# Performance work log

Hardware: AMD Instinct MI355X
Metric: run time of the kernel (lower is better)

The kernel has to match this reference:

```python
import jax, jax.numpy as jnp
import numpy as np

H = 64       # HIDDEN_DIM
NH = 2       # attention heads
HD = H // NH # head dim = 32
M = 8        # MEMORY_SLOTS
V = 64       # VOCAB_SIZE


def layer_norm(x, g, b):
    m = x.mean(-1, keepdims=True)
    v = ((x - m) ** 2).mean(-1, keepdims=True)
    return (x - m) / jnp.sqrt(v + 1e-5) * g + b


def mha(x, wi, bi, wo, bo):
    # torch nn.MultiheadAttention, batch_first, self-attention, avg head weights
    B, L, _ = x.shape
    qkv = x @ wi.T + bi                      # (B,L,3H)
    q, k, v = jnp.split(qkv, 3, axis=-1)
    q = q.reshape(B, L, NH, HD)
    k = k.reshape(B, L, NH, HD)
    v = v.reshape(B, L, NH, HD)
    s = jnp.einsum('bqhd,bkhd->bhqk', q, k) / jnp.sqrt(jnp.float32(HD))
    w = jax.nn.softmax(s, axis=-1)           # (B,NH,L,L)
    o = jnp.einsum('bhqk,bkhd->bqhd', w, v).reshape(B, L, H)
    return o @ wo.T + bo, w.mean(axis=1)     # averaged over heads


def ffn(x, w1, b1, w2, b2):
    return jax.nn.relu(x @ w1.T + b1) @ w2.T + b2


def setup_inputs() -> dict:
    key = jax.random.key(0)
    ks = iter(jax.random.split(key, 48))
    p = lambda shape: jax.random.normal(next(ks), shape, jnp.float32) * 0.02
    B, L = 16, 2048
    inp = {
        'seq': jax.random.randint(next(ks), (B, L), 0, V, jnp.int64 if jax.config.jax_enable_x64 else jnp.int32),
        'query': jax.random.randint(next(ks), (B,), 0, V, jnp.int32),
        'target': jax.random.randint(next(ks), (B,), 0, V, jnp.int32),
        'embed': p((V, H)),
        'a1_wi': p((3 * H, H)), 'a1_bi': p((3 * H,)), 'a1_wo': p((H, H)), 'a1_bo': p((H,)),
        'ff1_w1': p((2 * H, H)), 'ff1_b1': p((2 * H,)), 'ff1_w2': p((H, 2 * H)), 'ff1_b2': p((H,)),
        'ln1a_g': jnp.ones((H,)), 'ln1a_b': jnp.zeros((H,)),
        'ln1b_g': jnp.ones((H,)), 'ln1b_b': jnp.zeros((H,)),
        'a2_wi': p((3 * H, H)), 'a2_bi': p((3 * H,)), 'a2_wo': p((H, H)), 'a2_bo': p((H,)),
        'ff2_w1': p((2 * H, H)), 'ff2_b1': p((2 * H,)), 'ff2_w2': p((H, 2 * H)), 'ff2_b2': p((H,)),
        'ln2a_g': jnp.ones((H,)), 'ln2a_b': jnp.zeros((H,)),
        'ln2b_g': jnp.ones((H,)), 'ln2b_b': jnp.zeros((H,)),
        'rq_w': p((H, H)), 'rq_b': p((H,)),
        'ro_w': p((V, H)), 'ro_b': p((V,)),
        'qemb': p((V, H)),
    }
    return inp


def reference(seq, query, target, embed,
              a1_wi, a1_bi, a1_wo, a1_bo, ff1_w1, ff1_b1, ff1_w2, ff1_b2,
              ln1a_g, ln1a_b, ln1b_g, ln1b_b,
              a2_wi, a2_bi, a2_wo, a2_bo, ff2_w1, ff2_b1, ff2_w2, ff2_b2,
              ln2a_g, ln2a_b, ln2b_g, ln2b_b,
              rq_w, rq_b, ro_w, ro_b, qemb):
    # encoder
    h = embed[seq]                                        # (B,L,H)
    a1, _ = mha(h, a1_wi, a1_bi, a1_wo, a1_bo)
    h = layer_norm(h + a1, ln1a_g, ln1a_b)
    h = layer_norm(h + ffn(h, ff1_w1, ff1_b1, ff1_w2, ff1_b2), ln1b_g, ln1b_b)
    a2, attn_w = mha(h, a2_wi, a2_bi, a2_wo, a2_bo)       # attn_w: (B,L,L)
    h = layer_norm(h + a2, ln2a_g, ln2a_b)
    h = layer_norm(h + ffn(h, ff2_w1, ff2_b1, ff2_w2, ff2_b2), ln2b_g, ln2b_b)

    # slot selection (write_mode='attention'): per-key importance, top-k
    importance = attn_w.mean(axis=1)                      # (B,L)
    _, topk = jax.lax.top_k(importance, M)                # (B,M)
    mem = jnp.take_along_axis(h, topk[:, :, None], axis=1)  # (B,M,H)

    # memory reader
    q_h = qemb[query]                                     # (B,H)
    q = q_h @ rq_w.T + rq_b                               # (B,H)
    scores = (q[:, None, :] * mem).sum(-1) / jnp.sqrt(jnp.float32(H))  # (B,M)
    weights = jax.nn.softmax(scores, axis=-1)[:, :, None]
    read = (weights * mem).sum(1)                         # (B,H)
    logits = read @ ro_w.T + ro_b                         # (B,V)

    logp = jax.nn.log_softmax(logits, axis=-1)
    loss = -jnp.mean(logp[jnp.arange(logits.shape[0]), target])
    return loss, attn_w
```

## Files before the change

### kernel.cpp

```cpp
#include <hip/hip_runtime.h>
#include <hip/hip_bf16.h>


typedef unsigned short u16;
#define LQ 2048
#define BBATCH 16
#define QKB 262144

typedef __attribute__((ext_vector_type(8))) short bf16x8;
typedef __attribute__((ext_vector_type(4))) float f32x4;

__device__ __forceinline__ float bfu2f(u16 x){ return __uint_as_float(((unsigned)x) << 16); }
__device__ __forceinline__ u16 f2bu(float f){ return __bfloat16_as_ushort(__float2bfloat16(f)); }

__device__ __forceinline__ unsigned cvtpk(float lo, float hi){
  unsigned r;
  asm("v_cvt_pk_bf16_f32 %0, %1, %2" : "=v"(r) : "v"(lo), "v"(hi));
  return r;
}

__device__ __forceinline__ const u16* qk_rowp(const u16* qk_r15, const u16* qk_ws,
                                              int bz, int row){
  const u16* base = (bz < 15) ? (qk_r15 + (size_t)bz*QKB) : qk_ws;
  return base + (size_t)row*128;
}
__device__ __forceinline__ u16* qk_rowp_w(u16* qk_r15, u16* qk_ws, int bz, int row){
  u16* base = (bz < 15) ? (qk_r15 + (size_t)bz*QKB) : qk_ws;
  return base + (size_t)row*128;
}

__global__ __launch_bounds__(256) void k_embed(const int* __restrict__ seq,
                                               const float* __restrict__ emb,
                                               u16* __restrict__ h){
  int i = blockIdx.x*256 + threadIdx.x;
  int tok = i >> 6, d = i & 63;
  int v = seq[tok] & 63;
  h[i] = f2bu(emb[(v << 6) + d]);
}

__global__ __launch_bounds__(256) void k_zero(float* __restrict__ p, float* __restrict__ q){
  int i = blockIdx.x*256 + threadIdx.x;
  p[i] = 0.f;
  if (i == 0) q[0] = 0.f;
}

template<int MODE>
__global__ __launch_bounds__(256) void k_qkv(const u16* __restrict__ X,
                                             const float* __restrict__ W,
                                             const float* __restrict__ bias,
                                             u16* __restrict__ dqk0,
                                             u16* __restrict__ dqk_r15,
                                             u16* __restrict__ dqk_ws,
                                             u16* __restrict__ vg){
  __shared__ float WT[64*193];
  __shared__ float bs[192];
  const int t = threadIdx.x;
  for (int e=t; e<192*64; e+=256){ int mo=e>>6, k=e&63; WT[k*193+mo] = W[e]; }
  if (t < 192) bs[t] = bias[t];
  __syncthreads();
  const int wid=t>>6, lane=t&63;
  const int tok0 = (blockIdx.x*4 + wid)*4;
  float x[4];
  #pragma unroll
  for (int c=0;c<4;c++) x[c] = bfu2f(X[(tok0+c)*64 + lane]);
  float acc[4][3];
  #pragma unroll
  for (int c=0;c<4;c++)
    #pragma unroll
    for (int m=0;m<3;m++) acc[c][m] = bs[m*64 + lane];
  for (int k=0;k<64;k++){
    float wv[3];
    #pragma unroll
    for (int m=0;m<3;m++) wv[m] = WT[k*193 + m*64 + lane];
    #pragma unroll
    for (int c=0;c<4;c++){
      float xk = __shfl(x[c], k);
      #pragma unroll
      for (int m=0;m<3;m++) acc[c][m] += xk*wv[m];
    }
  }
  const float qs = 0.17677669529663688f;
  #pragma unroll
  for (int c=0;c<4;c++){
    int tok = tok0+c;
    float vq = acc[c][0]*qs, vk = acc[c][1], vv = acc[c][2];
    int b = tok >> 11, r = tok & 2047;
    u16* row = (MODE==0) ? (dqk0 + (size_t)tok*128) : qk_rowp_w(dqk_r15, dqk_ws, b, r);
    row[lane]      = f2bu(vq);
    row[64 + lane] = f2bu(vk);
    vg[((size_t)((b*64 + (r>>5))*4 + ((r>>2)&3))*64 + lane)*8
       + ((r>>4)&1)*4 + (r&3)] = f2bu(vv);
  }
}

template<int MODE>
__global__ __launch_bounds__(256, 4) void k_attn_ln(const u16* __restrict__ PQK,
    const u16* __restrict__ QKWS, const u16* __restrict__ VG,
    const float* __restrict__ wo, const float* __restrict__ bo,
    const float* __restrict__ g, const float* __restrict__ be,
    u16* __restrict__ h, float* __restrict__ lout){
  __shared__ float R[4096];
  __shared__ float ST[32*68];
  __shared__ float DN[2][32];
  __shared__ float CB[192];
  const int lin = blockIdx.x;
  const int nid = (lin & 7)*128 + (lin >> 3);
  const int qt = nid & 63, bz = nid >> 6;
  const int t = threadIdx.x;
  const int lane = t & 63, wv = t >> 6;
  const int n = lane & 15, gq = lane >> 4;
  const f32x4 FZ = {0.f, 0.f, 0.f, 0.f};

  for (int e=t; e<2048; e+=256) R[e] = 0.f;
  if (t < 64) DN[t>>5][t&31] = 0.f;
  __syncthreads();

  bf16x8 qf[2][2];
  #pragma unroll
  for (int qa=0; qa<2; qa++){
    const u16* qrow = (MODE==0) ? (PQK + (size_t)(bz*LQ + qt*32 + qa*16 + n)*128)
                                : qk_rowp(PQK, QKWS, bz, qt*32 + qa*16 + n);
    qf[qa][0] = *(const bf16x8*)(qrow + gq*8);
    qf[qa][1] = *(const bf16x8*)(qrow + 32 + gq*8);
  }
  f32x4 o[2][2][2];
  #pragma unroll
  for (int qa=0; qa<2; qa++)
    #pragma unroll
    for (int hh=0; hh<2; hh++)
      #pragma unroll
      for (int db=0; db<2; db++) o[qa][hh][db] = FZ;
  float dacc[2][2] = {{0.f,0.f},{0.f,0.f}};

  #pragma unroll 1
  for (int kt=wv*8; kt<wv*8+8; kt++){
    #pragma unroll
    for (int hh=0; hh<2; hh++){
      bf16x8 kf[4];
      #pragma unroll
      for (int jb=0; jb<4; jb++){
        const u16* kr = (MODE==0) ? (PQK + (size_t)(bz*LQ + kt*64 + jb*16 + n)*128)
                                  : qk_rowp(PQK, QKWS, bz, kt*64 + jb*16 + n);
        kf[jb] = *(const bf16x8*)(kr + 64 + hh*32 + gq*8);
      }
      unsigned pk[2][4][2];
      #pragma unroll
      for (int qa=0; qa<2; qa++){
        f32x4 ev[4];
        #pragma unroll
        for (int jb=0; jb<4; jb++)
          ev[jb] = __builtin_amdgcn_mfma_f32_16x16x32_bf16(kf[jb], qf[qa][hh], FZ, 0, 0, 0);
        float ds = 0.f;
        #pragma unroll
        for (int jb=0; jb<4; jb++){
          float e0 = __expf(ev[jb][0]), e1 = __expf(ev[jb][1]);
          float e2 = __expf(ev[jb][2]), e3 = __expf(ev[jb][3]);
          ds += (e0+e1) + (e2+e3);
          pk[qa][jb][0] = cvtpk(e0, e1);
          pk[qa][jb][1] = cvtpk(e2, e3);
        }
        dacc[qa][hh] += ds;
      }
      #pragma unroll
      for (int kb=0; kb<2; kb++){
        union { unsigned u[4]; bf16x8 v; } af[2];
        #pragma unroll
        for (int qa=0; qa<2; qa++){
          af[qa].u[0] = pk[qa][2*kb][0];   af[qa].u[1] = pk[qa][2*kb][1];
          af[qa].u[2] = pk[qa][2*kb+1][0]; af[qa].u[3] = pk[qa][2*kb+1][1];
        }
        #pragma unroll
        for (int db=0; db<2; db++){
          const int d = hh*32 + db*16 + n;
          const bf16x8 vf = *(const bf16x8*)(VG +
              ((size_t)((bz*64 + kt*2 + kb)*4 + gq)*64 + d)*8);
          #pragma unroll
          for (int qa=0; qa<2; qa++)
            o[qa][hh][db] = __builtin_amdgcn_mfma_f32_16x16x32_bf16(af[qa].v, vf, o[qa][hh][db], 0, 0, 0);
        }
      }
    }
  }
  #pragma unroll
  for (int qa=0; qa<2; qa++)
    #pragma unroll
    for (int hh=0; hh<2; hh++){
      float s = dacc[qa][hh];
      s += __shfl_xor(s, 16);
      s += __shfl_xor(s, 32);
      if (gq == 0) atomicAdd(&DN[hh][qa*16 + n], s);
    }
  #pragma unroll
  for (int qa=0; qa<2; qa++)
    #pragma unroll
    for (int hh=0; hh<2; hh++)
      #pragma unroll
      for (int db=0; db<2; db++)
        #pragma unroll
        for (int r=0; r<4; r++)
          atomicAdd(&R[(qa*16 + gq*4 + r)*64 + hh*32 + db*16 + n], o[qa][hh][db][r]);
  __syncthreads();
  if (lout && t < 64)
    lout[(size_t)(bz*2 + (t>>5))*LQ + qt*32 + (t&31)] = DN[t>>5][t&31];
  for (int e=t; e<2048; e+=256){
    int q = e >> 6, d = e & 63;
    ST[q*68 + d] = R[e] / DN[d>>5][q];
  }
  __syncthreads();
  for (int e2=t; e2<4096; e2+=256){ int k=e2>>6, mo=e2&63; R[e2] = wo[mo*64+k]; }
  if (t < 64)       CB[t] = bo[t];
  else if (t < 128) CB[t] = g[t-64];
  else if (t < 192) CB[t] = be[t-128];
  __syncthreads();
  for (int r=0; r<8; r++){
    int tl = wv*8 + r;
    size_t gtok = (size_t)(bz*LQ + qt*32 + tl);
    float acc = CB[lane];
    for (int k=0; k<64; k++) acc += ST[tl*68 + k] * R[k*64 + lane];
    float rr = acc + bfu2f(h[gtok*64 + lane]);
    float s = rr;
    #pragma unroll
    for (int ofs=32; ofs; ofs>>=1) s += __shfl_xor(s, ofs);
    float mean = s * (1.f/64.f);
    float dv = rr - mean;
    float vs = dv*dv;
    #pragma unroll
    for (int ofs=32; ofs; ofs>>=1) vs += __shfl_xor(vs, ofs);
    float rstd = 1.f/sqrtf(vs*(1.f/64.f) + 1e-5f);
    h[gtok*64 + lane] = f2bu(dv*rstd*CB[64+lane] + CB[128+lane]);
  }
}

__global__ __launch_bounds__(256) void k_ffn(u16* __restrict__ h,
    const float* __restrict__ w1, const float* __restrict__ b1,
    const float* __restrict__ w2, const float* __restrict__ b2,
    const float* __restrict__ g, const float* __restrict__ be){
  __shared__ u16 W1L[128*64];
  __shared__ u16 W2L[64*192];
  __shared__ u16 YL[64*64];
  __shared__ float B1[128], B2F[64], G[64], Bb[64];
  const int t = threadIdx.x;
  for (int e=t; e<8192; e+=256){
    int row = e>>6, col = e&63;
    W1L[row*64 + (col ^ ((row&7)<<3))] = f2bu(w1[e]);
  }
  for (int e=t; e<12288; e+=256){
    int o = e/192, rem = e%192, u = rem>>5, gs = rem&31, gq2 = gs>>3, s = gs&7;
    float val;
    if (u < 4) val = w2[o*128 + u*32 + ((s>>2)<<4) + gq2*4 + (s&3)];
    else { int d = ((u-4)<<5) + gq2*8 + s; val = (d==o) ? 1.f : 0.f; }
    W2L[o*192 + ((u*32+gs) ^ ((o&7)<<3))] = f2bu(val);
  }
  if (t < 128) B1[t] = b1[t];
  if (t < 64){ B2F[t] = b2[t]; G[t] = g[t]; Bb[t] = be[t]; }
  __syncthreads();
  const int lane = t & 63, wv = t >> 6;
  const int n = lane & 15, gq = lane >> 4;
  const int tok0 = blockIdx.x*64 + wv*16;
  bf16x8 xf[2];
  xf[0] = *(const bf16x8*)(h + (size_t)(tok0+n)*64 + gq*8);
  xf[1] = *(const bf16x8*)(h + (size_t)(tok0+n)*64 + 32 + gq*8);
  f32x4 acc1[8];
  #pragma unroll
  for (int ct=0; ct<8; ct++){
    f32x4 c;
    #pragma unroll
    for (int r=0;r<4;r++) c[r] = B1[ct*16 + gq*4 + r];
    bf16x8 w1f0 = *(const bf16x8*)(W1L + (ct*16+n)*64 + ((gq*8) ^ ((n&7)<<3)));
    bf16x8 w1f1 = *(const bf16x8*)(W1L + (ct*16+n)*64 + ((32+gq*8) ^ ((n&7)<<3)));
    c = __builtin_amdgcn_mfma_f32_16x16x32_bf16(w1f0, xf[0], c, 0, 0, 0);
    c = __builtin_amdgcn_mfma_f32_16x16x32_bf16(w1f1, xf[1], c, 0, 0, 0);
    acc1[ct] = c;
  }
  f32x4 acc2[4];
  #pragma unroll
  for (int ot=0; ot<4; ot++)
    #pragma unroll
    for (int r=0;r<4;r++) acc2[ot][r] = B2F[ot*16 + gq*4 + r];
  #pragma unroll
  for (int u=0; u<6; u++){
    union { unsigned uu[4]; bf16x8 v; } bfr;
    if (u < 4){
      #pragma unroll
      for (int i=0;i<4;i++){
        int ct = u*2 + (i>>1);
        float a = fmaxf(acc1[ct][(2*i)&3], 0.f);
        float b = fmaxf(acc1[ct][(2*i+1)&3], 0.f);
        bfr.uu[i] = (unsigned)f2bu(a) | ((unsigned)f2bu(b) << 16);
      }
    } else {
      bfr.v = xf[u-4];
    }
    #pragma unroll
    for (int ot=0; ot<4; ot++){
      bf16x8 w2f = *(const bf16x8*)(W2L + (ot*16+n)*192 + ((u*32+gq*8) ^ ((n&7)<<3)));
      acc2[ot] = __builtin_amdgcn_mfma_f32_16x16x32_bf16(w2f, bfr.v, acc2[ot], 0, 0, 0);
    }
  }
  float s1 = 0.f;
  #pragma unroll
  for (int ot=0;ot<4;ot++)
    #pragma unroll
    for (int r=0;r<4;r++) s1 += acc2[ot][r];
  s1 += __shfl_xor(s1, 16); s1 += __shfl_xor(s1, 32);
  float mean = s1 * (1.f/64.f);
  float s2 = 0.f;
  #pragma unroll
  for (int ot=0;ot<4;ot++)
    #pragma unroll
    for (int r=0;r<4;r++){ float dv = acc2[ot][r]-mean; s2 += dv*dv; }
  s2 += __shfl_xor(s2, 16); s2 += __shfl_xor(s2, 32);
  float rstd = 1.f/sqrtf(s2*(1.f/64.f) + 1e-5f);
  #pragma unroll
  for (int ot=0;ot<4;ot++)
    #pragma unroll
    for (int r=0;r<4;r++){
      int o = ot*16 + gq*4 + r;
      float yv = (acc2[ot][r]-mean)*rstd*G[o] + Bb[o];
      YL[(wv*16+n)*64 + (o ^ ((n&7)<<3))] = f2bu(yv);
    }
  __syncthreads();
  unsigned* h32 = (unsigned*)(h + (size_t)(blockIdx.x)*64*64);
  #pragma unroll
  for (int i=0;i<8;i++){
    int idx = i*64 + lane;
    int row = wv*16 + (idx>>5), c32 = idx&31;
    unsigned vv = *(const unsigned*)(YL + row*64 + ((c32*2) ^ ((row&7)<<3)));
    h32[row*32 + c32] = vv;
  }
}

__global__ __launch_bounds__(256) void k_imp(const u16* __restrict__ qk_r15,
    const u16* __restrict__ qk_ws, const float* __restrict__ l2,
    float* __restrict__ imp, int bz0){
  __shared__ float IMPS[256];
  __shared__ float INVL[128];
  const int t = threadIdx.x;
  const int qt = blockIdx.x >> 3, ks = blockIdx.x & 7;
  const int bz = bz0;
  const int lane = t & 63, wv = t >> 6;
  const int n = lane & 15, gq = lane >> 4;
  const f32x4 FZ = {0.f, 0.f, 0.f, 0.f};
  if (t < 128) INVL[t] = 1.f / l2[(size_t)(bz*2 + (t>>6))*LQ + qt*64 + (t&63)];
  IMPS[t] = 0.f;
  bf16x8 qf0, qf1;
  {
    const u16* qrow = qk_rowp(qk_r15, qk_ws, bz, qt*64 + wv*16 + n);
    qf0 = *(const bf16x8*)(qrow + gq*8);
    qf1 = *(const bf16x8*)(qrow + 32 + gq*8);
  }
  __syncthreads();
  float iv0[4], iv1[4];
  #pragma unroll
  for (int r=0;r<4;r++){
    iv0[r] = INVL[wv*16 + gq*4 + r];
    iv1[r] = INVL[64 + wv*16 + gq*4 + r];
  }
  for (int kt=ks*4; kt<ks*4+4; kt++){
    #pragma unroll
    for (int jb=0; jb<4; jb++){
      const u16* kr = qk_rowp(qk_r15, qk_ws, bz, kt*64 + jb*16 + n);
      bf16x8 kf0 = *(const bf16x8*)(kr + 64 + gq*8);
      bf16x8 kf1 = *(const bf16x8*)(kr + 96 + gq*8);
      f32x4 e0 = __builtin_amdgcn_mfma_f32_16x16x32_bf16(qf0, kf0, FZ, 0, 0, 0);
      f32x4 e1 = __builtin_amdgcn_mfma_f32_16x16x32_bf16(qf1, kf1, FZ, 0, 0, 0);
      float cs = 0.f;
      #pragma unroll
      for (int r=0;r<4;r++)
        cs += 0.5f*(__expf(e0[r])*iv0[r] + __expf(e1[r])*iv1[r]);
      cs += __shfl_xor(cs, 16);
      cs += __shfl_xor(cs, 32);
      if (gq == 0) atomicAdd(&IMPS[(kt-ks*4)*64 + jb*16 + n], cs);
    }
  }
  __syncthreads();
  atomicAdd(&imp[bz*LQ + ks*256 + t], IMPS[t]);
}

template<int DOIMP>
__global__ __launch_bounds__(256) void k_pass2(const u16* __restrict__ qk_r15,
    const u16* __restrict__ qk_ws, const float* __restrict__ l2,
    float* __restrict__ imp, float* __restrict__ wout, int bz0, int nper){
  __shared__ float STG[64*68];
  __shared__ float INVL[128];
  const int x = blockIdx.x;
  const int nid = (x & 7)*nper + (x >> 3);
  const int bz = bz0 + (nid >> 8);
  const int rem = nid & 255;
  const int qt = rem >> 3, ks = rem & 7;
  const int t = threadIdx.x;
  const int lane = t & 63, wv = t >> 6;
  const int n = lane & 15, gq = lane >> 4;
  const f32x4 FZ = {0.f, 0.f, 0.f, 0.f};
  if (t < 128) INVL[t] = 1.f / l2[(size_t)(bz*2 + (t>>6))*LQ + qt*64 + (t&63)];
  bf16x8 qf0, qf1;
  {
    const u16* qrow = qk_rowp(qk_r15, qk_ws, bz, qt*64 + wv*16 + n);
    qf0 = *(const bf16x8*)(qrow + gq*8);
    qf1 = *(const bf16x8*)(qrow + 32 + gq*8);
  }
  __syncthreads();
  const float iv0 = INVL[wv*16 + n], iv1 = INVL[64 + wv*16 + n];
  for (int kt = ks*4; kt < ks*4 + 4; kt++){
    #pragma unroll
    for (int jb=0; jb<4; jb++){
      const u16* kr = qk_rowp(qk_r15, qk_ws, bz, kt*64 + jb*16 + n);
      bf16x8 kf0 = *(const bf16x8*)(kr + 64 + gq*8);
      bf16x8 kf1 = *(const bf16x8*)(kr + 96 + gq*8);
      f32x4 e0 = __builtin_amdgcn_mfma_f32_16x16x32_bf16(kf0, qf0, FZ, 0, 0, 0);
      f32x4 e1 = __builtin_amdgcn_mfma_f32_16x16x32_bf16(kf1, qf1, FZ, 0, 0, 0);
      float4 w4;
      w4.x = 0.5f*(__expf(e0[0])*iv0 + __expf(e1[0])*iv1);
      w4.y = 0.5f*(__expf(e0[1])*iv0 + __expf(e1[1])*iv1);
      w4.z = 0.5f*(__expf(e0[2])*iv0 + __expf(e1[2])*iv1);
      w4.w = 0.5f*(__expf(e0[3])*iv0 + __expf(e1[3])*iv1);
      *(float4*)(&STG[(wv*16 + n)*68 + jb*16 + 4*gq]) = w4;
    }
    size_t base = 1 + (size_t)bz*LQ*LQ + (size_t)(qt*64)*LQ + (size_t)kt*64;
    float p = 0.f;
    for (int r=0; r<16; r++){
      int q = wv*16 + r;
      float v = STG[q*68 + lane];
      wout[base + (size_t)q*LQ + lane] = v;
      p += v;
    }
    if (DOIMP) atomicAdd(&imp[bz*LQ + kt*64 + lane], p);
  }
}

__global__ __launch_bounds__(64) void k_select(const float* __restrict__ imp,
    const u16* __restrict__ h,
    const int* __restrict__ query, const int* __restrict__ target,
    const float* __restrict__ qemb, const float* __restrict__ rq_w, const float* __restrict__ rq_b,
    const float* __restrict__ ro_w, const float* __restrict__ ro_b, float* __restrict__ out0){
  __shared__ float v[2048];
  __shared__ float bv[64];
  __shared__ int   bi[64];
  __shared__ int   chosen;
  __shared__ int   topi[8];
  const int b = blockIdx.x, lane = threadIdx.x;
  for (int i=lane; i<2048; i+=64) v[i] = imp[b*2048 + i];
  __syncthreads();
  for (int m=0; m<8; m++){
    float best = -1e30f; int besti = 1<<30;
    for (int i=lane; i<2048; i+=64)
      if (v[i] > best || (v[i] == best && i < besti)){ best = v[i]; besti = i; }
    bv[lane] = best; bi[lane] = besti;
    __syncthreads();
    if (lane == 0){
      float B = bv[0]; int I = bi[0];
      for (int i2=1; i2<64; i2++)
        if (bv[i2] > B || (bv[i2] == B && bi[i2] < I)){ B = bv[i2]; I = bi[i2]; }
      int c = (I < 0) ? 0 : (I > 2047 ? 2047 : I);
      topi[m] = c;
      chosen = c;
    }
    __syncthreads();
    if (lane == 0) v[chosen] = -1e30f;
    __syncthreads();
  }
  float mv[8];
  #pragma unroll
  for (int m=0; m<8; m++){
    int idx = topi[m] & 2047;
    mv[m] = bfu2f(h[(size_t)(b*LQ + idx)*64 + lane]);
  }
  float qh = qemb[((query[b]&63)<<6) + lane];
  float qd = rq_b[lane];
  for (int k=0;k<64;k++) qd += __shfl(qh,k) * rq_w[lane*64 + k];
  float sc[8];
  #pragma unroll
  for (int m=0;m<8;m++){
    float p = qd * mv[m];
    #pragma unroll
    for (int o=32;o;o>>=1) p += __shfl_xor(p,o);
    sc[m] = p * 0.125f;
  }
  float mx = sc[0];
  #pragma unroll
  for (int m=1;m<8;m++) mx = fmaxf(mx, sc[m]);
  float den = 0.f, rd = 0.f;
  #pragma unroll
  for (int m=0;m<8;m++){ float w = __expf(sc[m]-mx); den += w; rd += w*mv[m]; }
  rd /= den;
  float lg = ro_b[lane];
  for (int d=0;d<64;d++) lg += __shfl(rd,d) * ro_w[lane*64 + d];
  float lmx = lg;
  #pragma unroll
  for (int o=32;o;o>>=1) lmx = fmaxf(lmx, __shfl_xor(lmx,o));
  float ex = __expf(lg - lmx), es = ex;
  #pragma unroll
  for (int o=32;o;o>>=1) es += __shfl_xor(es,o);
  float lt = __shfl(lg, target[b]&63);
  if (lane == 0) atomicAdd(out0, -(lt - lmx - logf(es)) * (1.f/16.f));
}

extern "C" void kernel_launch(void* const* d_in, const int* in_sizes, int n_in,
                              void* d_out, int out_size, void* d_ws, size_t ws_size,
                              hipStream_t stream){
  const int*   seq    = (const int*)  d_in[0];
  const int*   query  = (const int*)  d_in[1];
  const int*   target = (const int*)  d_in[2];
  const float* embed  = (const float*)d_in[3];
  const float* a1_wi  = (const float*)d_in[4];
  const float* a1_bi  = (const float*)d_in[5];
  const float* a1_wo  = (const float*)d_in[6];
  const float* a1_bo  = (const float*)d_in[7];
  const float* ff1_w1 = (const float*)d_in[8];
  const float* ff1_b1 = (const float*)d_in[9];
  const float* ff1_w2 = (const float*)d_in[10];
  const float* ff1_b2 = (const float*)d_in[11];
  const float* ln1a_g = (const float*)d_in[12];
  const float* ln1a_b = (const float*)d_in[13];
  const float* ln1b_g = (const float*)d_in[14];
  const float* ln1b_b = (const float*)d_in[15];
  const float* a2_wi  = (const float*)d_in[16];
  const float* a2_bi  = (const float*)d_in[17];
  const float* a2_wo  = (const float*)d_in[18];
  const float* a2_bo  = (const float*)d_in[19];
  const float* ff2_w1 = (const float*)d_in[20];
  const float* ff2_b1 = (const float*)d_in[21];
  const float* ff2_w2 = (const float*)d_in[22];
  const float* ff2_b2 = (const float*)d_in[23];
  const float* ln2a_g = (const float*)d_in[24];
  const float* ln2a_b = (const float*)d_in[25];
  const float* ln2b_g = (const float*)d_in[26];
  const float* ln2b_b = (const float*)d_in[27];
  const float* rq_w   = (const float*)d_in[28];
  const float* rq_b   = (const float*)d_in[29];
  const float* ro_w   = (const float*)d_in[30];
  const float* ro_b   = (const float*)d_in[31];
  const float* qemb   = (const float*)d_in[32];

  char* wsb      = (char*)d_ws;
  u16*  qk_ws    = (u16*)(wsb);
  float* ws_imp  = (float*)(wsb + 524288);
  float* ws_l    = (float*)(wsb + 655360);

  float* out_f  = (float*)d_out;
  u16* qk1     = (u16*)((char*)d_out + 4194368);
  u16* vg1     = (u16*)((char*)d_out + 12582976);
  u16* vg2     = (u16*)((char*)d_out + 4194368);
  u16* qk_r15  = (u16*)((char*)d_out + 251658304);
  u16* h16     = (u16*)((char*)d_out + 259522624);

  k_embed<<<8192,256,0,stream>>>(seq, embed, h16);
  k_zero<<<128,256,0,stream>>>(ws_imp, out_f);
  k_qkv<0><<<2048,256,0,stream>>>(h16, a1_wi, a1_bi, qk1, nullptr, nullptr, vg1);
  k_attn_ln<0><<<1024,256,0,stream>>>(qk1, nullptr, vg1,
                                      a1_wo, a1_bo, ln1a_g, ln1a_b, h16, nullptr);
  k_ffn<<<512,256,0,stream>>>(h16, ff1_w1, ff1_b1, ff1_w2, ff1_b2, ln1b_g, ln1b_b);
  k_qkv<1><<<2048,256,0,stream>>>(h16, a2_wi, a2_bi, nullptr, qk_r15, qk_ws, vg2);
  k_attn_ln<1><<<1024,256,0,stream>>>(qk_r15, qk_ws, vg2,
                                      a2_wo, a2_bo, ln2a_g, ln2a_b, h16, ws_l);
  k_ffn<<<512,256,0,stream>>>(h16, ff2_w1, ff2_b1, ff2_w2, ff2_b2, ln2b_g, ln2b_b);
  k_pass2<1><<<3840,256,0,stream>>>(qk_r15, qk_ws, ws_l, ws_imp, out_f, 0, 480);
  k_imp<<<256,256,0,stream>>>(qk_r15, qk_ws, ws_l, ws_imp, 15);
  k_select<<<16,64,0,stream>>>(ws_imp, h16, query, target, qemb,
                               rq_w, rq_b, ro_w, ro_b, out_f);
  k_pass2<0><<<256,256,0,stream>>>(qk_r15, qk_ws, ws_l, nullptr, out_f, 15, 32);
}
```

Measured before the change: 838.1 us.

## Use MFMA for QKV projection, fold zeroing into embed, partial importance sums

The QKV projection moves from a scalar FMA loop with shuffles to bf16 MFMA tiles of 64 tokens per block. Output is staged in LDS so Q/K rows and the V layout can be written with wider coalesced stores. The zero-init kernel is merged into the embed kernel. In pass2, importance partials accumulate in shared memory and go to a per-query-tile buffer that k_select reduces, replacing global atomics. The attention-weight stores become nontemporal. Risks: bf16 rounding of weights, and extra reads in k_select.

```diff
diff --git a/kernel.cpp b/kernel.cpp
--- a/kernel.cpp
+++ b/kernel.cpp
@@ -31,17 +31,15 @@
 
 __global__ __launch_bounds__(256) void k_embed(const int* __restrict__ seq,
                                                const float* __restrict__ emb,
-                                               u16* __restrict__ h){
+                                               u16* __restrict__ h,
+                                               float* __restrict__ imp0,
+                                               float* __restrict__ out0){
   int i = blockIdx.x*256 + threadIdx.x;
+  if (i < 32768) imp0[i] = 0.f;
+  if (i == 0) out0[0] = 0.f;
   int tok = i >> 6, d = i & 63;
   int v = seq[tok] & 63;
   h[i] = f2bu(emb[(v << 6) + d]);
-}
-
-__global__ __launch_bounds__(256) void k_zero(float* __restrict__ p, float* __restrict__ q){
-  int i = blockIdx.x*256 + threadIdx.x;
-  p[i] = 0.f;
-  if (i == 0) q[0] = 0.f;
 }
 
 template<int MODE>
@@ -52,44 +50,62 @@
                                              u16* __restrict__ dqk_r15,
                                              u16* __restrict__ dqk_ws,
                                              u16* __restrict__ vg){
-  __shared__ float WT[64*193];
-  __shared__ float bs[192];
+  __shared__ u16 WL[192*64];
+  __shared__ unsigned YL32[64*97];
+  __shared__ float BS[192];
   const int t = threadIdx.x;
-  for (int e=t; e<192*64; e+=256){ int mo=e>>6, k=e&63; WT[k*193+mo] = W[e]; }
-  if (t < 192) bs[t] = bias[t];
-  __syncthreads();
-  const int wid=t>>6, lane=t&63;
-  const int tok0 = (blockIdx.x*4 + wid)*4;
-  float x[4];
-  #pragma unroll
-  for (int c=0;c<4;c++) x[c] = bfu2f(X[(tok0+c)*64 + lane]);
-  float acc[4][3];
-  #pragma unroll
-  for (int c=0;c<4;c++)
-    #pragma unroll
-    for (int m=0;m<3;m++) acc[c][m] = bs[m*64 + lane];
-  for (int k=0;k<64;k++){
-    float wv[3];
-    #pragma unroll
-    for (int m=0;m<3;m++) wv[m] = WT[k*193 + m*64 + lane];
-    #pragma unroll
-    for (int c=0;c<4;c++){
-      float xk = __shfl(x[c], k);
-      #pragma unroll
-      for (int m=0;m<3;m++) acc[c][m] += xk*wv[m];
-    }
-  }
+  for (int e=t; e<12288; e+=256){
+    int m = e>>6, k = e&63;
+    WL[m*64 + (k ^ ((m&7)<<3))] = f2bu(W[e]);
+  }
+  if (t < 192) BS[t] = bias[t];
+  __syncthreads();
+  const int lane = t & 63, wv = t >> 6;
+  const int n = lane & 15, gq = lane >> 4;
+  const int tok0 = blockIdx.x*64;
+  const int tl = wv*16 + n;
+  bf16x8 xf0 = *(const bf16x8*)(X + (size_t)(tok0+tl)*64 + gq*8);
+  bf16x8 xf1 = *(const bf16x8*)(X + (size_t)(tok0+tl)*64 + 32 + gq*8);
   const float qs = 0.17677669529663688f;
   #pragma unroll
-  for (int c=0;c<4;c++){
-    int tok = tok0+c;
-    float vq = acc[c][0]*qs, vk = acc[c][1], vv = acc[c][2];
-    int b = tok >> 11, r = tok & 2047;
-    u16* row = (MODE==0) ? (dqk0 + (size_t)tok*128) : qk_rowp_w(dqk_r15, dqk_ws, b, r);
-    row[lane]      = f2bu(vq);
-    row[64 + lane] = f2bu(vk);
-    vg[((size_t)((b*64 + (r>>5))*4 + ((r>>2)&3))*64 + lane)*8
-       + ((r>>4)&1)*4 + (r&3)] = f2bu(vv);
+  for (int ct=0; ct<12; ct++){
+    f32x4 c;
+    #pragma unroll
+    for (int r=0;r<4;r++) c[r] = BS[ct*16 + gq*4 + r];
+    bf16x8 wf0 = *(const bf16x8*)(WL + (ct*16+n)*64 + ((gq*8) ^ ((n&7)<<3)));
+    bf16x8 wf1 = *(const bf16x8*)(WL + (ct*16+n)*64 + ((32+gq*8) ^ ((n&7)<<3)));
+    c = __builtin_amdgcn_mfma_f32_16x16x32_bf16(wf0, xf0, c, 0, 0, 0);
+    c = __builtin_amdgcn_mfma_f32_16x16x32_bf16(wf1, xf1, c, 0, 0, 0);
+    if (ct < 4){ c[0]*=qs; c[1]*=qs; c[2]*=qs; c[3]*=qs; }
+    YL32[tl*97 + ct*8 + gq*2]     = cvtpk(c[0], c[1]);
+    YL32[tl*97 + ct*8 + gq*2 + 1] = cvtpk(c[2], c[3]);
+  }
+  __syncthreads();
+  const int b = tok0 >> 11, rbase = tok0 & 2047;
+  #pragma unroll
+  for (int i=0;i<16;i++){
+    int idx = i*256 + t;
+    int rl = idx>>6, cc = idx&63;
+    u16* row = (MODE==0) ? (dqk0 + (size_t)(tok0+rl)*128)
+                         : qk_rowp_w(dqk_r15, dqk_ws, b, rbase+rl);
+    ((unsigned*)row)[cc] = YL32[rl*97 + cc];
+  }
+  #pragma unroll
+  for (int i=0;i<4;i++){
+    int gid = i*256 + t;
+    int grp = gid>>6, d = gid&63;
+    int j0 = rbase + grp*4;
+    unsigned lohi[2];
+    #pragma unroll
+    for (int p=0;p<2;p++){
+      unsigned w0 = YL32[(grp*4 + 2*p)*97 + 64 + (d>>1)];
+      unsigned w1 = YL32[(grp*4 + 2*p + 1)*97 + 64 + (d>>1)];
+      u16 a  = (d&1) ? (u16)(w0>>16) : (u16)(w0 & 0xffffu);
+      u16 bb = (d&1) ? (u16)(w1>>16) : (u16)(w1 & 0xffffu);
+      lohi[p] = (unsigned)a | ((unsigned)bb << 16);
+    }
+    size_t A = ((size_t)((b*64 + (j0>>5))*4 + ((j0>>2)&3))*64 + d)*8 + ((j0>>4)&1)*4;
+    *(uint2*)(vg + A) = make_uint2(lohi[0], lohi[1]);
   }
 }
 
@@ -380,9 +396,10 @@
 template<int DOIMP>
 __global__ __launch_bounds__(256) void k_pass2(const u16* __restrict__ qk_r15,
     const u16* __restrict__ qk_ws, const float* __restrict__ l2,
-    float* __restrict__ imp, float* __restrict__ wout, int bz0, int nper){
+    float* __restrict__ part, float* __restrict__ wout, int bz0, int nper){
   __shared__ float STG[64*68];
   __shared__ float INVL[128];
+  __shared__ float PIMP[256];
   const int x = blockIdx.x;
   const int nid = (x & 7)*nper + (x >> 3);
   const int bz = bz0 + (nid >> 8);
@@ -393,6 +410,7 @@
   const int n = lane & 15, gq = lane >> 4;
   const f32x4 FZ = {0.f, 0.f, 0.f, 0.f};
   if (t < 128) INVL[t] = 1.f / l2[(size_t)(bz*2 + (t>>6))*LQ + qt*64 + (t&63)];
+  if (DOIMP) PIMP[t] = 0.f;
   bf16x8 qf0, qf1;
   {
     const u16* qrow = qk_rowp(qk_r15, qk_ws, bz, qt*64 + wv*16 + n);
@@ -421,15 +439,19 @@
     for (int r=0; r<16; r++){
       int q = wv*16 + r;
       float v = STG[q*68 + lane];
-      wout[base + (size_t)q*LQ + lane] = v;
+      __builtin_nontemporal_store(v, &wout[base + (size_t)q*LQ + lane]);
       p += v;
     }
-    if (DOIMP) atomicAdd(&imp[bz*LQ + kt*64 + lane], p);
-  }
-}
-
-__global__ __launch_bounds__(64) void k_select(const float* __restrict__ imp,
-    const u16* __restrict__ h,
+    if (DOIMP) atomicAdd(&PIMP[(kt-ks*4)*64 + lane], p);
+  }
+  if (DOIMP){
+    __syncthreads();
+    part[((size_t)qt*16 + bz)*LQ + ks*256 + t] = PIMP[t];
+  }
+}
+
+__global__ __launch_bounds__(64) void k_select(const float* __restrict__ imp15,
+    const float* __restrict__ part, const u16* __restrict__ h,
     const int* __restrict__ query, const int* __restrict__ target,
     const float* __restrict__ qemb, const float* __restrict__ rq_w, const float* __restrict__ rq_b,
     const float* __restrict__ ro_w, const float* __restrict__ ro_b, float* __restrict__ out0){
@@ -439,7 +461,17 @@
   __shared__ int   chosen;
   __shared__ int   topi[8];
   const int b = blockIdx.x, lane = threadIdx.x;
-  for (int i=lane; i<2048; i+=64) v[i] = imp[b*2048 + i];
+  for (int i=lane; i<2048; i+=64){
+    float s;
+    if (b < 15){
+      s = 0.f;
+      #pragma unroll 4
+      for (int qt=0; qt<32; qt++) s += part[((size_t)qt*16 + b)*LQ + i];
+    } else {
+      s = imp15[b*2048 + i];
+    }
+    v[i] = s;
+  }
   __syncthreads();
   for (int m=0; m<8; m++){
     float best = -1e30f; int besti = 1<<30;
@@ -543,20 +575,20 @@
   u16* vg2     = (u16*)((char*)d_out + 4194368);
   u16* qk_r15  = (u16*)((char*)d_out + 251658304);
   u16* h16     = (u16*)((char*)d_out + 259522624);
-
-  k_embed<<<8192,256,0,stream>>>(seq, embed, h16);
-  k_zero<<<128,256,0,stream>>>(ws_imp, out_f);
-  k_qkv<0><<<2048,256,0,stream>>>(h16, a1_wi, a1_bi, qk1, nullptr, nullptr, vg1);
+  float* Ppart = (float*)((char*)d_out + 263716928);
+
+  k_embed<<<8192,256,0,stream>>>(seq, embed, h16, ws_imp, out_f);
+  k_qkv<0><<<512,256,0,stream>>>(h16, a1_wi, a1_bi, qk1, nullptr, nullptr, vg1);
   k_attn_ln<0><<<1024,256,0,stream>>>(qk1, nullptr, vg1,
                                       a1_wo, a1_bo, ln1a_g, ln1a_b, h16, nullptr);
   k_ffn<<<512,256,0,stream>>>(h16, ff1_w1, ff1_b1, ff1_w2, ff1_b2, ln1b_g, ln1b_b);
-  k_qkv<1><<<2048,256,0,stream>>>(h16, a2_wi, a2_bi, nullptr, qk_r15, qk_ws, vg2);
+  k_qkv<1><<<512,256,0,stream>>>(h16, a2_wi, a2_bi, nullptr, qk_r15, qk_ws, vg2);
   k_attn_ln<1><<<1024,256,0,stream>>>(qk_r15, qk_ws, vg2,
                                       a2_wo, a2_bo, ln2a_g, ln2a_b, h16, ws_l);
   k_ffn<<<512,256,0,stream>>>(h16, ff2_w1, ff2_b1, ff2_w2, ff2_b2, ln2b_g, ln2b_b);
-  k_pass2<1><<<3840,256,0,stream>>>(qk_r15, qk_ws, ws_l, ws_imp, out_f, 0, 480);
+  k_pass2<1><<<3840,256,0,stream>>>(qk_r15, qk_ws, ws_l, Ppart, out_f, 0, 480);
   k_imp<<<256,256,0,stream>>>(qk_r15, qk_ws, ws_l, ws_imp, 15);
-  k_select<<<16,64,0,stream>>>(ws_imp, h16, query, target, qemb,
+  k_select<<<16,64,0,stream>>>(ws_imp, Ppart, h16, query, target, qemb,
                                rq_w, rq_b, ro_w, ro_b, out_f);
   k_pass2<0><<<256,256,0,stream>>>(qk_r15, qk_ws, ws_l, nullptr, out_f, 15, 32);
 }
```

Result: slower. 892.6 us (+6.5%).
